# Performance work log

Measured on AMD Instinct MI355X. Metric: run time of the kernel, lower is better.

Reference implementation:

```python
import jax, jax.numpy as jnp
import numpy as np
from jax import lax

E = 1e-13            # WENO smoothness epsilon
MULT_BIAS = 0.1      # weno5_mult_bias
PADS = (2, 2, 0, 0, 1, 0)


def _conv1d(x, w, b, pad):
    # x: [1, Cin, N], w: [Cout, Cin, K], b: [Cout]
    y = lax.conv_general_dilated(x, w, window_strides=(1,), padding=[(pad, pad)],
                                 dimension_numbers=('NCH', 'OIH', 'NCH'))
    return y + b[None, :, None]


def _cnn(dif, params):
    # inner_nn_weno5: 5 Conv+ELU blocks then Conv+Sigmoid; dif: [N]
    x = dif[None, None, :]
    for i in range(6):
        x = _conv1d(x, params[2 * i], params[2 * i + 1], PADS[i])
        x = jax.nn.elu(x) if i < 5 else jax.nn.sigmoid(x)
    return x[0, 0]  # [N]


def _avg_diff(uu):
    # __get_average_diff: average of left/right forward differences, edges replicated
    d = uu[1:] - uu[:-1]                       # [N-1]
    d_left = jnp.concatenate([d, d[-1:]])      # [N]
    d_right = jnp.concatenate([d[:1], d])      # [N]
    return 0.5 * (d_left + d_right)


def _weno5(uu, params):
    # w5_minus=True, mweno=True, mapped=False, trainable=True
    def fluxes(u):
        um, umm = jnp.roll(u, 1), jnp.roll(u, 2)
        up, upp = jnp.roll(u, -1), jnp.roll(u, -2)
        f0 = (11 * u - 7 * up + 2 * upp) / 6
        f1 = (2 * um + 5 * u - up) / 6
        f2 = (-umm + 5 * um + 2 * u) / 6
        return f0, f1, f2

    def betas(u):
        um, umm = jnp.roll(u, 1), jnp.roll(u, 2)
        up, upp = jnp.roll(u, -1), jnp.roll(u, -2)
        b0 = 13 / 12 * (u - 2 * up + upp) ** 2 + 0.25 * (3 * u - 4 * up + upp) ** 2
        b1 = 13 / 12 * (um - 2 * u + up) ** 2 + 0.25 * (um - up) ** 2
        b2 = 13 / 12 * (umm - 2 * um + u) ** 2 + 0.25 * (umm - 4 * um + 3 * u) ** 2
        return b0, b1, b2

    u_right = jnp.roll(uu, -1)
    fp = fluxes(u_right)
    fn = fluxes(uu)
    bp = list(betas(u_right))
    bn = list(betas(uu))

    # trainable beta correction from the small CNN flux limiter
    bm = _cnn(_avg_diff(uu), params) + MULT_BIAS
    bp = [b * jnp.roll(bm, k - 1) for k, b in enumerate(bp)]
    bn = [b * jnp.roll(bm, k - 1) for k, b in enumerate(bn)]

    ds = (0.1, 0.6, 0.3)

    def omegas(bs):  # mweno=True variant, then normalize
        brs = (bs[2] - bs[0]) ** 2
        om = [d / (E + b) ** 2 * (brs + (E + b) ** 2) for b, d in zip(bs, ds)]
        s = om[0] + om[1] + om[2]
        return [o / s for o in om]

    op = omegas(bp)
    on = omegas(bn)
    fluxp = op[0] * fp[0] + op[1] * fp[1] + op[2] * fp[2]
    fluxn = on[0] * fn[0] + on[1] * fn[1] + on[2] * fn[2]
    return fluxp - fluxn


def setup_inputs() -> dict:
    key = jax.random.key(0)
    ks = jax.random.split(key, 13)
    N = 2097152
    uu = jax.random.normal(ks[0], (N,), dtype=jnp.float32)
    shapes = [(20, 1, 5), (40, 20, 5), (80, 40, 1), (40, 80, 1), (20, 40, 3), (1, 20, 1)]
    inp = {'uu': uu}
    for i, (co, ci, k) in enumerate(shapes):
        fan_in = ci * k
        scale = jnp.float32(1.0 / np.sqrt(fan_in))
        inp[f'w{i + 1}'] = jax.random.normal(ks[2 * i + 1], (co, ci, k), dtype=jnp.float32) * scale
        inp[f'b{i + 1}'] = jax.random.normal(ks[2 * i + 2], (co,), dtype=jnp.float32) * 0.01
    return inp


def reference(uu, w1, b1, w2, b2, w3, b3, w4, b4, w5, b5, w6, b6):
    params = (w1, b1, w2, b2, w3, b3, w4, b4, w5, b5, w6, b6)
    return _weno5(uu, params)
```

## Files before the change

kernel.cpp:

```cpp
#include <hip/hip_runtime.h>
#include <cstdint>

#define N_PTS 2097152
#define MASK  (N_PTS - 1)

constexpr int NPOS = 128;
constexpr int POUT = 116;
constexpr int GOFF = 6;
constexpr int BLK  = 256;
constexpr int NBLK = (N_PTS + POUT - 1) / POUT;

constexpr int ST1 = 40;
constexpr int ST2 = 56;
constexpr int ST4 = 56;

constexpr int SLOTA_OFF = 0;
constexpr int SLOTA_SZ  = 14576;
constexpr int SLOTB_OFF = SLOTA_SZ;
constexpr int SLOTB_SZ  = 14352;
constexpr int TAIL_OFF  = SLOTB_OFF + SLOTB_SZ;
constexpr int SMEM_BYTES = TAIL_OFF + 392 * 4;

constexpr int F2 = 0;
constexpr int F3 = 7680;
constexpr int F4 = 12800;
constexpr int F5 = 17408;
constexpr int F1 = 23552;
constexpr int NFRAG2 = 15, NFRAG3 = 10, NFRAG4 = 9, NFRAG5 = 12;
constexpr int NPREP = NFRAG2 + NFRAG3 + NFRAG4 + NFRAG5 + 2;
constexpr int BME_OFF = 65536;

constexpr float L2E = 1.4426950408889634f;
constexpr float LN2 = 0.6931471805599453f;

typedef _Float16 f16x8 __attribute__((ext_vector_type(8)));
typedef _Float16 f16x2 __attribute__((ext_vector_type(2)));
typedef unsigned short u16x8 __attribute__((ext_vector_type(8)));
typedef float f32x4 __attribute__((ext_vector_type(4)));

constexpr unsigned short F16_ONE = 0x3C00;

extern "C" __device__ _Float16 __ocml_exp2_f16(_Float16);

__device__ __forceinline__ float fastrcp(float x) {
#if __has_builtin(__builtin_amdgcn_rcpf)
    return __builtin_amdgcn_rcpf(x);
#else
    return 1.f / x;
#endif
}

__device__ __forceinline__ float fastexp2(float x) {
#if __has_builtin(__builtin_amdgcn_exp2f)
    return __builtin_amdgcn_exp2f(x);
#else
    return __expf(x * LN2);
#endif
}

__device__ __forceinline__ float elu_t(float t) {
    const float e = fastexp2(fminf(t, 0.f));
    return fmaxf(t, fmaf(e, L2E, -L2E));
}

__device__ __forceinline__ unsigned short f2h_rtne(float f) {
    return __builtin_bit_cast(unsigned short, (_Float16)f);
}

__device__ __forceinline__ unsigned int elu2_pk(float t0, float t1) {
    f16x2 h = __builtin_bit_cast(f16x2, __builtin_amdgcn_cvt_pkrtz(t0, t1));
    const f16x2 z = {(_Float16)0.f, (_Float16)0.f};
    f16x2 m = __builtin_elementwise_min(h, z);
    f16x2 e;
    e[0] = __ocml_exp2_f16(m[0]);
    e[1] = __ocml_exp2_f16(m[1]);
    const f16x2 l2e2  = {(_Float16)L2E, (_Float16)L2E};
    const f16x2 nl2e2 = {(_Float16)(-L2E), (_Float16)(-L2E)};
    f16x2 el = __builtin_elementwise_fma(e, l2e2, nl2e2);
    f16x2 r = __builtin_elementwise_max(h, el);
    return __builtin_bit_cast(unsigned int, r);
}

__device__ __forceinline__ unsigned int cvt_pkrtz_u(float lo, float hi) {
    return __builtin_bit_cast(unsigned int, __builtin_amdgcn_cvt_pkrtz(lo, hi));
}

template<int M, int MT, int CI, int KS, int KT>
__device__ __forceinline__ void pack_one(const float* __restrict__ W,
                                         const float* __restrict__ Bias, int biasTap,
                                         unsigned short* __restrict__ dst,
                                         int f, int lane)
{
    const int ks = f % KS;
    const int fi = f / KS;
    const int mt = fi % MT;
    const int t  = fi / MT;
    const int m  = mt * 16 + (lane & 15);
    const int kb = ks * 32 + (lane >> 4) * 8;
    u16x8 v;
    #pragma unroll
    for (int j = 0; j < 8; ++j) {
        const int k = kb + j;
        float val = 0.f;
        if (m < M) {
            if (k < CI)                          val = W[(m * CI + k) * KT + t];
            else if (k == CI && t == biasTap)    val = Bias[m] * L2E;
        }
        v[j] = f2h_rtne(val);
    }
    *(u16x8*)(dst + (f * 64 + lane) * 8) = v;
}

__global__ __launch_bounds__(64) void prep_kernel(
    const float* __restrict__ w1, const float* __restrict__ b1,
    const float* __restrict__ w2, const float* __restrict__ b2,
    const float* __restrict__ w3, const float* __restrict__ b3,
    const float* __restrict__ w4, const float* __restrict__ b4,
    const float* __restrict__ w5, const float* __restrict__ b5,
    unsigned short* __restrict__ frags,
    float* __restrict__ bmE)
{
    const int lane = threadIdx.x;
    const int b = blockIdx.x;
    if (b == 0 && lane < 4) bmE[lane] = 0.f;
    if (b < NFRAG2)
        pack_one<40, 3, 20, 1, 5>(w2, b2, 2, frags + F2, b, lane);
    else if (b < NFRAG2 + NFRAG3)
        pack_one<80, 5, 40, 2, 1>(w3, b3, 0, frags + F3, b - NFRAG2, lane);
    else if (b < NFRAG2 + NFRAG3 + NFRAG4) {
        const int f  = b - NFRAG2 - NFRAG3;
        const int ks = f % 3;
        const int mt = f / 3;
        const int m  = mt * 16 + (lane & 15);
        const int q  = lane >> 4;
        u16x8 v;
        #pragma unroll
        for (int j = 0; j < 8; ++j) {
            float val = 0.f;
            if (m < 40) {
                if (ks < 2) {
                    const int ch = ks * 32 + ((j >> 2) << 4) + q * 4 + (j & 3);
                    val = w4[m * 80 + ch];
                } else if (j < 4) {
                    const int ch = 64 + q * 4 + j;
                    val = w4[m * 80 + ch];
                } else if (j == 4 && q == 0) {
                    val = b4[m] * L2E;
                }
            }
            v[j] = f2h_rtne(val);
        }
        *(u16x8*)(frags + F4 + (f * 64 + lane) * 8) = v;
    }
    else if (b < NFRAG2 + NFRAG3 + NFRAG4 + NFRAG5)
        pack_one<20, 2, 40, 2, 3>(w5, b5, 1, frags + F5, b - NFRAG2 - NFRAG3 - NFRAG4, lane);
    else {
        const int mt = b - (NPREP - 2);
        const int m  = mt * 16 + (lane & 15);
        const int kb = (lane >> 4) * 8;
        u16x8 v;
        #pragma unroll
        for (int j = 0; j < 8; ++j) {
            const int k = kb + j;
            float val = 0.f;
            if (m < 20) {
                if (k < 5)      val = w1[m * 5 + k] * L2E;
                else if (k == 5) val = b1[m] * L2E;
            }
            v[j] = f2h_rtne(val);
        }
        *(u16x8*)(frags + F1 + (mt * 64 + lane) * 8) = v;
    }
}

template<int NF>
__device__ __forceinline__ void load_A(const unsigned short* __restrict__ Af,
                                       int lane, f16x8* A) {
    #pragma unroll
    for (int f = 0; f < NF; ++f)
        A[f] = __builtin_bit_cast(f16x8, *(const u16x8*)(Af + (f * 64 + lane) * 8));
}

template<int TAPS, int MT, int KS, typename Epi>
__device__ __forceinline__ void gemm_tap(const unsigned short* __restrict__ Af,
                                         const unsigned short* __restrict__ Bbuf,
                                         int SB, f32x4 Z4, Epi epi)
{
    const int lane = threadIdx.x & 63;
    const int wv   = threadIdx.x >> 6;
    const int n15  = lane & 15;
    const int quad = lane >> 4;

    f16x8 A[TAPS * MT * KS];
    load_A<TAPS * MT * KS>(Af, lane, A);

    f16x8 B[2][TAPS][KS];
    #pragma unroll
    for (int nt = 0; nt < 2; ++nt) {
        const int pos = (wv * 2 + nt) * 16 + n15;
        #pragma unroll
        for (int t = 0; t < TAPS; ++t)
            #pragma unroll
            for (int ks = 0; ks < KS; ++ks)
                B[nt][t][ks] = __builtin_bit_cast(f16x8,
                    *(const u16x8*)(Bbuf + (pos + t) * SB + ks * 32 + quad * 8));
    }

    #pragma unroll
    for (int nt = 0; nt < 2; ++nt) {
        const int pos = (wv * 2 + nt) * 16 + n15;
        #pragma unroll
        for (int mt = 0; mt < MT; ++mt) {
            f32x4 acc = __builtin_amdgcn_mfma_f32_16x16x32_f16(
                A[mt * KS], B[nt][0][0], Z4, 0, 0, 0);
            #pragma unroll
            for (int i = 1; i < TAPS * KS; ++i) {
                const int t = i / KS, ks = i - t * KS;
                acc = __builtin_amdgcn_mfma_f32_16x16x32_f16(
                    A[(t * MT + mt) * KS + ks], B[nt][t][ks], acc, 0, 0, 0);
            }
            epi(mt, pos, acc);
        }
    }
}

__device__ __forceinline__ float weno_math(float um2, float um1, float u0,
                                           float up1, float up2, float up3,
                                           float bmm, float bm0, float bmp)
{
    const float c1312 = 13.f / 12.f;
    const float s6 = 1.f / 6.f;

    const float f0p = (11.f * up1 - 7.f * up2 + 2.f * up3) * s6;
    const float f1p = (2.f * u0 + 5.f * up1 - up2) * s6;
    const float f2p = (-um1 + 5.f * u0 + 2.f * up1) * s6;
    const float f0n = (11.f * u0 - 7.f * up1 + 2.f * up2) * s6;
    const float f1n = (2.f * um1 + 5.f * u0 - up1) * s6;
    const float f2n = (-um2 + 5.f * um1 + 2.f * u0) * s6;

    float t0, t1;
    t0 = up1 - 2.f * up2 + up3;  t1 = 3.f * up1 - 4.f * up2 + up3;
    float bp0 = c1312 * t0 * t0 + 0.25f * t1 * t1;
    t0 = u0 - 2.f * up1 + up2;   t1 = u0 - up2;
    float bp1 = c1312 * t0 * t0 + 0.25f * t1 * t1;
    t0 = um1 - 2.f * u0 + up1;   t1 = um1 - 4.f * u0 + 3.f * up1;
    float bp2 = c1312 * t0 * t0 + 0.25f * t1 * t1;
    t0 = u0 - 2.f * up1 + up2;   t1 = 3.f * u0 - 4.f * up1 + up2;
    float bn0 = c1312 * t0 * t0 + 0.25f * t1 * t1;
    t0 = um1 - 2.f * u0 + up1;   t1 = um1 - up1;
    float bn1 = c1312 * t0 * t0 + 0.25f * t1 * t1;
    t0 = um2 - 2.f * um1 + u0;   t1 = um2 - 4.f * um1 + 3.f * u0;
    float bn2 = c1312 * t0 * t0 + 0.25f * t1 * t1;

    bp0 *= bmp; bp1 *= bm0; bp2 *= bmm;
    bn0 *= bmp; bn1 *= bm0; bn2 *= bmm;

    const float E = 1e-13f;
    float brs, e, r0, r1, r2, o0, o1, o2;

    brs = bp2 - bp0; brs *= brs;
    e = E + bp0; e *= e; r0 = fastrcp(e);
    e = E + bp1; e *= e; r1 = fastrcp(e);
    e = E + bp2; e *= e; r2 = fastrcp(e);
    o0 = 0.1f * fmaf(brs, r0, 1.f);
    o1 = 0.6f * fmaf(brs, r1, 1.f);
    o2 = 0.3f * fmaf(brs, r2, 1.f);
    const float fluxp = (o0 * f0p + o1 * f1p + o2 * f2p) * fastrcp(o0 + o1 + o2);

    brs = bn2 - bn0; brs *= brs;
    e = E + bn0; e *= e; r0 = fastrcp(e);
    e = E + bn1; e *= e; r1 = fastrcp(e);
    e = E + bn2; e *= e; r2 = fastrcp(e);
    o0 = 0.1f * fmaf(brs, r0, 1.f);
    o1 = 0.6f * fmaf(brs, r1, 1.f);
    o2 = 0.3f * fmaf(brs, r2, 1.f);
    const float fluxn = (o0 * f0n + o1 * f1n + o2 * f2n) * fastrcp(o0 + o1 + o2);

    return fluxp - fluxn;
}

__global__ __launch_bounds__(BLK, 5) void cnn_weno_kernel(
    const float* __restrict__ u,
    const float* __restrict__ w6, const float* __restrict__ b6,
    const unsigned short* __restrict__ frags,
    float* __restrict__ bmE,
    float* __restrict__ out)
{
    if (blockIdx.x == NBLK) {
        if (threadIdx.x == 0) {
            float b0, b1, b2, b3;
            for (;;) {
                b0 = __hip_atomic_load(&bmE[0], __ATOMIC_ACQUIRE, __HIP_MEMORY_SCOPE_AGENT);
                b1 = __hip_atomic_load(&bmE[1], __ATOMIC_ACQUIRE, __HIP_MEMORY_SCOPE_AGENT);
                b2 = __hip_atomic_load(&bmE[2], __ATOMIC_ACQUIRE, __HIP_MEMORY_SCOPE_AGENT);
                b3 = __hip_atomic_load(&bmE[3], __ATOMIC_ACQUIRE, __HIP_MEMORY_SCOPE_AGENT);
                if (b0 != 0.f && b1 != 0.f && b2 != 0.f && b3 != 0.f) break;
                __builtin_amdgcn_s_sleep(2);
            }
            out[0] = weno_math(u[N_PTS - 2], u[N_PTS - 1], u[0],
                               u[1], u[2], u[3], b3, b0, b1);
            out[N_PTS - 1] = weno_math(u[N_PTS - 3], u[N_PTS - 2], u[N_PTS - 1],
                                       u[0], u[1], u[2], b2, b3, b0);
        }
        return;
    }

    extern __shared__ char smem[];
    unsigned short* act1 = (unsigned short*)(smem + SLOTA_OFF);
    unsigned short* act4 = (unsigned short*)(smem + SLOTA_OFF);
    unsigned short* act2 = (unsigned short*)(smem + SLOTB_OFF);
    float* sdif = (float*)(smem + TAIL_OFF);
    float* sw6  = sdif + 132;
    float* sb6  = sw6 + 20;
    float* sbm  = sb6 + 1;
    float* su   = sbm + 118;

    const int tid  = threadIdx.x;
    const int lane = tid & 63;
    const int wv   = tid >> 6;
    const int n15  = lane & 15;
    const int quad = lane >> 4;
    const int i0   = blockIdx.x * POUT;
    const bool edge = (blockIdx.x == 0) || (blockIdx.x >= NBLK - 1);

    const f32x4 Z4 = {0.f, 0.f, 0.f, 0.f};

    {
        const u16x8 z8 = {0, 0, 0, 0, 0, 0, 0, 0};
        for (int r = tid; r < 130; r += BLK)
            *(u16x8*)(act4 + r * ST4 + 48) = z8;
        for (int r = tid; r < 128; r += BLK)
            *(u16x8*)(act2 + r * ST2 + 48) = z8;
        if (tid < 20)       *(u16x8*)(act1 + 128 * ST1 + tid * 8) = z8;
        else if (tid == 20) *(u16x8*)(act2 + 128 * ST2) = z8;
        else if (tid < 27)  *(u16x8*)(act4 + 129 * ST4 + (tid - 21) * 8) = z8;
        else if (tid == 27) *(u16x8*)(act4 + 130 * ST4) = z8;
        else if (tid < 34)  *(u16x8*)(act4 + (tid - 28) * 8) = z8;
    }
    if (!edge) {
        for (int d = tid; d < 132; d += BLK) {
            const int g = i0 - 10 + d;
            sdif[d] = 0.5f * (u[g + 1] - u[g - 1]);
        }
        for (int j = tid; j < 121; j += BLK)
            su[j] = u[i0 - 2 + j];
    } else {
        for (int d = tid; d < 132; d += BLK) {
            const int g = i0 - 10 + d;
            float v = 0.f;
            if (g >= 0 && g < N_PTS) {
                if (g == 0)              v = u[1] - u[0];
                else if (g == N_PTS - 1) v = u[N_PTS - 1] - u[N_PTS - 2];
                else                     v = 0.5f * (u[g + 1] - u[g - 1]);
            }
            sdif[d] = v;
        }
        for (int j = tid; j < 121; j += BLK)
            su[j] = u[(i0 - 2 + j) & MASK];
    }
    if (tid < 20)       sw6[tid] = w6[tid] * LN2;
    else if (tid == 20) sb6[0] = b6[0];
    __syncthreads();

    {
        f16x8 A1[2];
        load_A<2>(frags + F1, lane, A1);
        float s[2][5];
        #pragma unroll
        for (int nt = 0; nt < 2; ++nt) {
            const int pos = (wv * 2 + nt) * 16 + n15;
            #pragma unroll
            for (int j = 0; j < 5; ++j)
                s[nt][j] = sdif[pos + j];
        }
        #pragma unroll
        for (int nt = 0; nt < 2; ++nt) {
            const int pos = (wv * 2 + nt) * 16 + n15;
            uint4 bd;
            bd.x = cvt_pkrtz_u(s[nt][0], s[nt][1]);
            bd.y = cvt_pkrtz_u(s[nt][2], s[nt][3]);
            bd.z = cvt_pkrtz_u(s[nt][4], 1.0f);
            bd.w = 0u;
            const f16x8 B = __builtin_bit_cast(f16x8, bd);
            const f32x4 a0 = __builtin_amdgcn_mfma_f32_16x16x32_f16(A1[0], B, Z4, 0, 0, 0);
            const f32x4 a1 = __builtin_amdgcn_mfma_f32_16x16x32_f16(A1[1], B, Z4, 0, 0, 0);
            bool oor = false;
            if (edge) {
                const int g = i0 + pos - 8;
                oor = ((unsigned)g >= (unsigned)N_PTS);
            }
            {
                uint2 w;
                w.x = elu2_pk(a0[0], a0[1]); w.y = elu2_pk(a0[2], a0[3]);
                if (oor) { w.x = 0u; w.y = 0u; }
                *(uint2*)(act1 + pos * ST1 + quad * 4) = w;
            }
            {
                uint2 w;
                if (quad == 0) {
                    w.x = elu2_pk(a1[0], a1[1]); w.y = elu2_pk(a1[2], a1[3]);
                    if (oor) { w.x = 0u; w.y = 0u; }
                } else if (quad == 1) {
                    w.x = (unsigned)F16_ONE; w.y = 0u;
                } else {
                    w.x = 0u; w.y = 0u;
                }
                *(uint2*)(act1 + pos * ST1 + 16 + quad * 4) = w;
            }
        }
    }
    __syncthreads();

    gemm_tap<5, 3, 1>(frags + F2, act1, ST1, Z4,
        [&](int mt, int pos, f32x4 acc) {
            const int ch0 = mt * 16 + quad * 4;
            unsigned short* dst = act2 + pos * ST2 + ch0;
            if (mt < 2 || quad < 2) {
                uint2 w;
                w.x = elu2_pk(acc[0], acc[1]); w.y = elu2_pk(acc[2], acc[3]);
                if (edge) {
                    const int g = i0 - GOFF + pos;
                    if ((unsigned)g >= (unsigned)N_PTS) { w.x = 0u; w.y = 0u; }
                }
                *(uint2*)dst = w;
            } else {
                uint2 w; w.x = (quad == 2) ? (unsigned)F16_ONE : 0u; w.y = 0u;
                *(uint2*)dst = w;
            }
        });
    __syncthreads();

    {
        unsigned int p[2][5][2];
        {
            f16x8 A3[10];
            load_A<10>(frags + F3, lane, A3);
            f16x8 B3[2][2];
            #pragma unroll
            for (int nt = 0; nt < 2; ++nt) {
                const int pos = (wv * 2 + nt) * 16 + n15;
                #pragma unroll
                for (int ks = 0; ks < 2; ++ks)
                    B3[nt][ks] = __builtin_bit_cast(f16x8,
                        *(const u16x8*)(act2 + pos * ST2 + ks * 32 + quad * 8));
            }
            #pragma unroll
            for (int nt = 0; nt < 2; ++nt) {
                #pragma unroll
                for (int mt = 0; mt < 5; ++mt) {
                    f32x4 acc = __builtin_amdgcn_mfma_f32_16x16x32_f16(
                        A3[mt * 2 + 0], B3[nt][0], Z4, 0, 0, 0);
                    acc = __builtin_amdgcn_mfma_f32_16x16x32_f16(
                        A3[mt * 2 + 1], B3[nt][1], acc, 0, 0, 0);
                    p[nt][mt][0] = elu2_pk(acc[0], acc[1]);
                    p[nt][mt][1] = elu2_pk(acc[2], acc[3]);
                }
            }
        }
        {
            f16x8 A4[9];
            load_A<9>(frags + F4, lane, A4);
            const unsigned int biasw = (quad == 0) ? (unsigned)F16_ONE : 0u;
            #pragma unroll
            for (int nt = 0; nt < 2; ++nt) {
                const int pos = (wv * 2 + nt) * 16 + n15;
                uint4 w0, w1, w2;
                w0.x = p[nt][0][0]; w0.y = p[nt][0][1]; w0.z = p[nt][1][0]; w0.w = p[nt][1][1];
                w1.x = p[nt][2][0]; w1.y = p[nt][2][1]; w1.z = p[nt][3][0]; w1.w = p[nt][3][1];
                w2.x = p[nt][4][0]; w2.y = p[nt][4][1]; w2.z = biasw;       w2.w = 0u;
                f16x8 B4[3];
                B4[0] = __builtin_bit_cast(f16x8, w0);
                B4[1] = __builtin_bit_cast(f16x8, w1);
                B4[2] = __builtin_bit_cast(f16x8, w2);
                #pragma unroll
                for (int mt = 0; mt < 3; ++mt) {
                    f32x4 acc = __builtin_amdgcn_mfma_f32_16x16x32_f16(
                        A4[mt * 3 + 0], B4[0], Z4, 0, 0, 0);
                    acc = __builtin_amdgcn_mfma_f32_16x16x32_f16(
                        A4[mt * 3 + 1], B4[1], acc, 0, 0, 0);
                    acc = __builtin_amdgcn_mfma_f32_16x16x32_f16(
                        A4[mt * 3 + 2], B4[2], acc, 0, 0, 0);
                    const int ch0 = mt * 16 + quad * 4;
                    unsigned short* dst = act4 + (pos + 1) * ST4 + ch0;
                    if (mt < 2 || quad < 2) {
                        uint2 w;
                        w.x = elu2_pk(acc[0], acc[1]); w.y = elu2_pk(acc[2], acc[3]);
                        if (edge) {
                            const int g = i0 - GOFF + pos;
                            if ((unsigned)g >= (unsigned)N_PTS) { w.x = 0u; w.y = 0u; }
                        }
                        *(uint2*)dst = w;
                    } else {
                        uint2 w; w.x = (quad == 2) ? (unsigned)F16_ONE : 0u; w.y = 0u;
                        *(uint2*)dst = w;
                    }
                }
            }
        }
    }
    __syncthreads();

    {
        f16x8 A5[12];
        load_A<12>(frags + F5, lane, A5);
        #pragma unroll
        for (int nt = 0; nt < 2; ++nt) {
            const int pos = (wv * 2 + nt) * 16 + n15;
            f16x8 B[3][2];
            #pragma unroll
            for (int t = 0; t < 3; ++t)
                #pragma unroll
                for (int ks = 0; ks < 2; ++ks)
                    B[t][ks] = __builtin_bit_cast(f16x8,
                        *(const u16x8*)(act4 + (pos + t) * ST4 + ks * 32 + quad * 8));
            f32x4 a0 = __builtin_amdgcn_mfma_f32_16x16x32_f16(A5[0], B[0][0], Z4, 0, 0, 0);
            f32x4 a1 = __builtin_amdgcn_mfma_f32_16x16x32_f16(A5[2], B[0][0], Z4, 0, 0, 0);
            #pragma unroll
            for (int i = 1; i < 6; ++i) {
                const int t = i >> 1, ks = i & 1;
                a0 = __builtin_amdgcn_mfma_f32_16x16x32_f16(
                    A5[(t * 2 + 0) * 2 + ks], B[t][ks], a0, 0, 0, 0);
                a1 = __builtin_amdgcn_mfma_f32_16x16x32_f16(
                    A5[(t * 2 + 1) * 2 + ks], B[t][ks], a1, 0, 0, 0);
            }
            float partial = 0.f;
            const int c0 = quad * 4;
            #pragma unroll
            for (int r = 0; r < 4; ++r)
                partial += sw6[c0 + r] * elu_t(a0[r]);
            if (quad == 0) {
                #pragma unroll
                for (int r = 0; r < 4; ++r)
                    partial += sw6[16 + r] * elu_t(a1[r]);
            }
            partial += __shfl_xor(partial, 16, 64);
            partial += __shfl_xor(partial, 32, 64);
            if (quad == 0) {
                const float bmv = fastrcp(1.f + __expf(-(partial + sb6[0]))) + 0.1f;
                if (pos >= 5 && pos < 123) sbm[pos - 5] = bmv;
                if (edge) {
                    const int g = i0 - GOFF + pos;
                    if (blockIdx.x == 0) {
                        if (g == 0)
                            __hip_atomic_store(&bmE[0], bmv, __ATOMIC_RELEASE, __HIP_MEMORY_SCOPE_AGENT);
                        else if (g == 1)
                            __hip_atomic_store(&bmE[1], bmv, __ATOMIC_RELEASE, __HIP_MEMORY_SCOPE_AGENT);
                    }
                    if (blockIdx.x == NBLK - 1) {
                        if (g == N_PTS - 2)
                            __hip_atomic_store(&bmE[2], bmv, __ATOMIC_RELEASE, __HIP_MEMORY_SCOPE_AGENT);
                        else if (g == N_PTS - 1)
                            __hip_atomic_store(&bmE[3], bmv, __ATOMIC_RELEASE, __HIP_MEMORY_SCOPE_AGENT);
                    }
                }
            }
        }
    }
    __syncthreads();

    if (tid < POUT) {
        const int g = i0 + tid;
        if (g < N_PTS && g != 0 && g != N_PTS - 1) {
            out[g] = weno_math(su[tid], su[tid + 1], su[tid + 2],
                               su[tid + 3], su[tid + 4], su[tid + 5],
                               sbm[tid], sbm[tid + 1], sbm[tid + 2]);
        }
    }
}

extern "C" void kernel_launch(void* const* d_in, const int* in_sizes, int n_in,
                              void* d_out, int out_size, void* d_ws, size_t ws_size,
                              hipStream_t stream) {
    const float* u  = (const float*)d_in[0];
    const float* w1 = (const float*)d_in[1];
    const float* b1 = (const float*)d_in[2];
    const float* w2 = (const float*)d_in[3];
    const float* b2 = (const float*)d_in[4];
    const float* w3 = (const float*)d_in[5];
    const float* b3 = (const float*)d_in[6];
    const float* w4 = (const float*)d_in[7];
    const float* b4 = (const float*)d_in[8];
    const float* w5 = (const float*)d_in[9];
    const float* b5 = (const float*)d_in[10];
    const float* w6 = (const float*)d_in[11];
    const float* b6 = (const float*)d_in[12];

    unsigned short* frags = (unsigned short*)d_ws;
    float* bmE = (float*)((char*)d_ws + BME_OFF);

    (void)hipFuncSetAttribute((const void*)cnn_weno_kernel,
                              hipFuncAttributeMaxDynamicSharedMemorySize,
                              SMEM_BYTES);

    prep_kernel<<<NPREP, 64, 0, stream>>>(w1, b1, w2, b2, w3, b3, w4, b4, w5, b5,
                                          frags, bmE);
    cnn_weno_kernel<<<NBLK + 1, BLK, SMEM_BYTES, stream>>>(u, w6, b6, frags, bmE,
                                                           (float*)d_out);
}
```

Baseline: 244.3 us.

## Inject conv3/conv5 biases via MFMA accumulator init to shrink LDS rows

Layers 3 and 5 no longer fold their bias into the weight fragments through an extra constant-one input channel. Instead the biases (pre-scaled by log2 e) go into a small table and are loaded as the initial MFMA accumulator. The ones-channel padding in the layer-2 and layer-4 activation rows is no longer needed, so their LDS stride drops from 56 to 40 halfs, and the launch bound is raised from 5 to 7 blocks per CU. This targets LDS-limited occupancy and some padding and ones-channel stores. It risks more bank conflicts at the narrower stride and tighter register limits.

Result: slower. 345.5 us (+41.4%).

```diff
diff --git a/kernel.cpp b/kernel.cpp
--- a/kernel.cpp
+++ b/kernel.cpp
@@ -11,14 +11,15 @@
 constexpr int NBLK = (N_PTS + POUT - 1) / POUT;
 
 constexpr int ST1 = 40;
-constexpr int ST2 = 56;
-constexpr int ST4 = 56;
+constexpr int ST2 = 40;
+constexpr int ST4 = 40;
 
 constexpr int SLOTA_OFF = 0;
-constexpr int SLOTA_SZ  = 14576;
+constexpr int SLOTA_SZ  = 10560;
 constexpr int SLOTB_OFF = SLOTA_SZ;
-constexpr int SLOTB_SZ  = 14352;
-constexpr int TAIL_OFF  = SLOTB_OFF + SLOTB_SZ;
+constexpr int SLOTB_SZ  = 10320;
+constexpr int SBIAS_OFF = SLOTA_SZ + SLOTB_SZ;
+constexpr int TAIL_OFF  = SBIAS_OFF + 100 * 4;
 constexpr int SMEM_BYTES = TAIL_OFF + 392 * 4;
 
 constexpr int F2 = 0;
@@ -28,6 +29,7 @@
 constexpr int F1 = 23552;
 constexpr int NFRAG2 = 15, NFRAG3 = 10, NFRAG4 = 9, NFRAG5 = 12;
 constexpr int NPREP = NFRAG2 + NFRAG3 + NFRAG4 + NFRAG5 + 2;
+constexpr int BIAS_OFF = 49152;
 constexpr int BME_OFF = 65536;
 
 constexpr float L2E = 1.4426950408889634f;
@@ -118,15 +120,22 @@
     const float* __restrict__ w4, const float* __restrict__ b4,
     const float* __restrict__ w5, const float* __restrict__ b5,
     unsigned short* __restrict__ frags,
+    float* __restrict__ biasT,
     float* __restrict__ bmE)
 {
     const int lane = threadIdx.x;
     const int b = blockIdx.x;
-    if (b == 0 && lane < 4) bmE[lane] = 0.f;
+    if (b == 0) {
+        if (lane < 4) bmE[lane] = 0.f;
+        for (int i = lane; i < 100; i += 64) {
+            const float v = (i < 80) ? b3[i] : b5[i - 80];
+            biasT[i] = v * L2E;
+        }
+    }
     if (b < NFRAG2)
         pack_one<40, 3, 20, 1, 5>(w2, b2, 2, frags + F2, b, lane);
     else if (b < NFRAG2 + NFRAG3)
-        pack_one<80, 5, 40, 2, 1>(w3, b3, 0, frags + F3, b - NFRAG2, lane);
+        pack_one<80, 5, 40, 2, 1>(w3, b3, -1, frags + F3, b - NFRAG2, lane);
     else if (b < NFRAG2 + NFRAG3 + NFRAG4) {
         const int f  = b - NFRAG2 - NFRAG3;
         const int ks = f % 3;
@@ -153,7 +162,7 @@
         *(u16x8*)(frags + F4 + (f * 64 + lane) * 8) = v;
     }
     else if (b < NFRAG2 + NFRAG3 + NFRAG4 + NFRAG5)
-        pack_one<20, 2, 40, 2, 3>(w5, b5, 1, frags + F5, b - NFRAG2 - NFRAG3 - NFRAG4, lane);
+        pack_one<20, 2, 40, 2, 3>(w5, b5, -1, frags + F5, b - NFRAG2 - NFRAG3 - NFRAG4, lane);
     else {
         const int mt = b - (NPREP - 2);
         const int m  = mt * 16 + (lane & 15);
@@ -279,10 +288,11 @@
     return fluxp - fluxn;
 }
 
-__global__ __launch_bounds__(BLK, 5) void cnn_weno_kernel(
+__global__ __launch_bounds__(BLK, 7) void cnn_weno_kernel(
     const float* __restrict__ u,
     const float* __restrict__ w6, const float* __restrict__ b6,
     const unsigned short* __restrict__ frags,
+    const float* __restrict__ biasTg,
     float* __restrict__ bmE,
     float* __restrict__ out)
 {
@@ -309,6 +319,7 @@
     unsigned short* act1 = (unsigned short*)(smem + SLOTA_OFF);
     unsigned short* act4 = (unsigned short*)(smem + SLOTA_OFF);
     unsigned short* act2 = (unsigned short*)(smem + SLOTB_OFF);
+    float* sbias = (float*)(smem + SBIAS_OFF);
     float* sdif = (float*)(smem + TAIL_OFF);
     float* sw6  = sdif + 132;
     float* sb6  = sw6 + 20;
@@ -327,15 +338,10 @@
 
     {
         const u16x8 z8 = {0, 0, 0, 0, 0, 0, 0, 0};
-        for (int r = tid; r < 130; r += BLK)
-            *(u16x8*)(act4 + r * ST4 + 48) = z8;
-        for (int r = tid; r < 128; r += BLK)
-            *(u16x8*)(act2 + r * ST2 + 48) = z8;
         if (tid < 20)       *(u16x8*)(act1 + 128 * ST1 + tid * 8) = z8;
-        else if (tid == 20) *(u16x8*)(act2 + 128 * ST2) = z8;
-        else if (tid < 27)  *(u16x8*)(act4 + 129 * ST4 + (tid - 21) * 8) = z8;
-        else if (tid == 27) *(u16x8*)(act4 + 130 * ST4) = z8;
-        else if (tid < 34)  *(u16x8*)(act4 + (tid - 28) * 8) = z8;
+        else if (tid < 23)  *(u16x8*)(act2 + 128 * ST2 + (tid - 20) * 8) = z8;
+        else if (tid < 28)  *(u16x8*)(act4 + (tid - 23) * 8) = z8;
+        if (tid < 100) sbias[tid] = biasTg[tid];
     }
     if (!edge) {
         for (int d = tid; d < 132; d += BLK) {
@@ -413,8 +419,6 @@
 
     gemm_tap<5, 3, 1>(frags + F2, act1, ST1, Z4,
         [&](int mt, int pos, f32x4 acc) {
-            const int ch0 = mt * 16 + quad * 4;
-            unsigned short* dst = act2 + pos * ST2 + ch0;
             if (mt < 2 || quad < 2) {
                 uint2 w;
                 w.x = elu2_pk(acc[0], acc[1]); w.y = elu2_pk(acc[2], acc[3]);
@@ -422,10 +426,7 @@
                     const int g = i0 - GOFF + pos;
                     if ((unsigned)g >= (unsigned)N_PTS) { w.x = 0u; w.y = 0u; }
                 }
-                *(uint2*)dst = w;
-            } else {
-                uint2 w; w.x = (quad == 2) ? (unsigned)F16_ONE : 0u; w.y = 0u;
-                *(uint2*)dst = w;
+                *(uint2*)(act2 + pos * ST2 + mt * 16 + quad * 4) = w;
             }
         });
     __syncthreads();
@@ -445,11 +446,12 @@
                         *(const u16x8*)(act2 + pos * ST2 + ks * 32 + quad * 8));
             }
             #pragma unroll
-            for (int nt = 0; nt < 2; ++nt) {
+            for (int mt = 0; mt < 5; ++mt) {
+                const f32x4 c3 = *(const f32x4*)(sbias + mt * 16 + quad * 4);
                 #pragma unroll
-                for (int mt = 0; mt < 5; ++mt) {
+                for (int nt = 0; nt < 2; ++nt) {
                     f32x4 acc = __builtin_amdgcn_mfma_f32_16x16x32_f16(
-                        A3[mt * 2 + 0], B3[nt][0], Z4, 0, 0, 0);
+                        A3[mt * 2 + 0], B3[nt][0], c3, 0, 0, 0);
                     acc = __builtin_amdgcn_mfma_f32_16x16x32_f16(
                         A3[mt * 2 + 1], B3[nt][1], acc, 0, 0, 0);
                     p[nt][mt][0] = elu2_pk(acc[0], acc[1]);
@@ -480,8 +482,6 @@
                         A4[mt * 3 + 1], B4[1], acc, 0, 0, 0);
                     acc = __builtin_amdgcn_mfma_f32_16x16x32_f16(
                         A4[mt * 3 + 2], B4[2], acc, 0, 0, 0);
-                    const int ch0 = mt * 16 + quad * 4;
-                    unsigned short* dst = act4 + (pos + 1) * ST4 + ch0;
                     if (mt < 2 || quad < 2) {
                         uint2 w;
                         w.x = elu2_pk(acc[0], acc[1]); w.y = elu2_pk(acc[2], acc[3]);
@@ -489,10 +489,7 @@
                             const int g = i0 - GOFF + pos;
                             if ((unsigned)g >= (unsigned)N_PTS) { w.x = 0u; w.y = 0u; }
                         }
-                        *(uint2*)dst = w;
-                    } else {
-                        uint2 w; w.x = (quad == 2) ? (unsigned)F16_ONE : 0u; w.y = 0u;
-                        *(uint2*)dst = w;
+                        *(uint2*)(act4 + (pos + 1) * ST4 + mt * 16 + quad * 4) = w;
                     }
                 }
             }
@@ -503,6 +500,8 @@
     {
         f16x8 A5[12];
         load_A<12>(frags + F5, lane, A5);
+        const f32x4 c0 = *(const f32x4*)(sbias + 80 + quad * 4);
+        const f32x4 c1 = *(const f32x4*)(sbias + 80 + 16);
         #pragma unroll
         for (int nt = 0; nt < 2; ++nt) {
             const int pos = (wv * 2 + nt) * 16 + n15;
@@ -513,8 +512,8 @@
                 for (int ks = 0; ks < 2; ++ks)
                     B[t][ks] = __builtin_bit_cast(f16x8,
                         *(const u16x8*)(act4 + (pos + t) * ST4 + ks * 32 + quad * 8));
-            f32x4 a0 = __builtin_amdgcn_mfma_f32_16x16x32_f16(A5[0], B[0][0], Z4, 0, 0, 0);
-            f32x4 a1 = __builtin_amdgcn_mfma_f32_16x16x32_f16(A5[2], B[0][0], Z4, 0, 0, 0);
+            f32x4 a0 = __builtin_amdgcn_mfma_f32_16x16x32_f16(A5[0], B[0][0], c0, 0, 0, 0);
+            f32x4 a1 = __builtin_amdgcn_mfma_f32_16x16x32_f16(A5[2], B[0][0], c1, 0, 0, 0);
             #pragma unroll
             for (int i = 1; i < 6; ++i) {
                 const int t = i >> 1, ks = i & 1;
@@ -524,10 +523,10 @@
                     A5[(t * 2 + 1) * 2 + ks], B[t][ks], a1, 0, 0, 0);
             }
             float partial = 0.f;
-            const int c0 = quad * 4;
+            const int c0i = quad * 4;
             #pragma unroll
             for (int r = 0; r < 4; ++r)
-                partial += sw6[c0 + r] * elu_t(a0[r]);
+                partial += sw6[c0i + r] * elu_t(a0[r]);
             if (quad == 0) {
                 #pragma unroll
                 for (int r = 0; r < 4; ++r)
@@ -586,6 +585,7 @@
     const float* b6 = (const float*)d_in[12];
 
     unsigned short* frags = (unsigned short*)d_ws;
+    float* biasT = (float*)((char*)d_ws + BIAS_OFF);
     float* bmE = (float*)((char*)d_ws + BME_OFF);
 
     (void)hipFuncSetAttribute((const void*)cnn_weno_kernel,
@@ -593,7 +593,7 @@
                               SMEM_BYTES);
 
     prep_kernel<<<NPREP, 64, 0, stream>>>(w1, b1, w2, b2, w3, b3, w4, b4, w5, b5,
-                                          frags, bmE);
-    cnn_weno_kernel<<<NBLK + 1, BLK, SMEM_BYTES, stream>>>(u, w6, b6, frags, bmE,
-                                                           (float*)d_out);
-}
+                                          frags, biasT, bmE);
+    cnn_weno_kernel<<<NBLK + 1, BLK, SMEM_BYTES, stream>>>(u, w6, b6, frags, biasT,
+                                                           bmE, (float*)d_out);
+}
```
